# Optimization experiments

Measured on AMD Instinct MI355X. Metric: run time of the kernel, lower is better.

## Reference

```python
import jax, jax.numpy as jnp
import numpy as np

N = 20000
E = 320000
DIN = 256
DH = 64
DOUT = 64
H = 8
NEG_SLOPE = 0.2


def _glorot(key, shape):
    fan_in, fan_out = shape[0], shape[-1]
    lim = jnp.sqrt(6.0 / (fan_in + fan_out))
    return jax.random.uniform(key, shape, jnp.float32, -lim, lim)


def setup_inputs() -> dict:
    key = jax.random.key(0)
    ks = jax.random.split(key, 12)
    x = jax.random.normal(ks[0], (N, DIN), jnp.float32)
    edge_index = jax.random.randint(ks[1], (2, E), 0, N, jnp.int32)
    # layer 1: dim_in -> heads*dim_h
    Wl1 = _glorot(ks[2], (DIN, H * DH));  bl1 = jnp.zeros((H * DH,), jnp.float32)
    Wr1 = _glorot(ks[3], (DIN, H * DH));  br1 = jnp.zeros((H * DH,), jnp.float32)
    att1 = _glorot(ks[4], (H, DH))
    bias1 = jnp.zeros((H * DH,), jnp.float32)
    # layer 2: heads*dim_h -> heads*dim_out
    Wl2 = _glorot(ks[5], (H * DH, H * DOUT)); bl2 = jnp.zeros((H * DOUT,), jnp.float32)
    Wr2 = _glorot(ks[6], (H * DH, H * DOUT)); br2 = jnp.zeros((H * DOUT,), jnp.float32)
    att2 = _glorot(ks[7], (H, DOUT))
    bias2 = jnp.zeros((H * DOUT,), jnp.float32)
    return dict(x=x, edge_index=edge_index, Wl1=Wl1, bl1=bl1, Wr1=Wr1, br1=br1,
                att1=att1, bias1=bias1, Wl2=Wl2, bl2=bl2, Wr2=Wr2, br2=br2,
                att2=att2, bias2=bias2)


def _gatv2(x, src, dst, Wl, bl, Wr, br, att, bias_out, heads, out_ch):
    n = x.shape[0]
    l = (x @ Wl + bl).reshape(n, heads, out_ch)   # source transform
    r = (x @ Wr + br).reshape(n, heads, out_ch)   # target transform
    # per-edge GATv2 score: att . LeakyReLU(l_j + r_i)
    e = jax.nn.leaky_relu(l[src] + r[dst], NEG_SLOPE)      # [E, H, C]
    logits = jnp.einsum('ehc,hc->eh', e, att)              # [E, H]
    # segmented softmax over incoming edges of each destination node
    m = jax.ops.segment_max(logits, dst, num_segments=n)   # [N, H]
    expd = jnp.exp(logits - m[dst])
    denom = jax.ops.segment_sum(expd, dst, num_segments=n)
    alpha = expd / denom[dst]                              # [E, H]
    msg = l[src] * alpha[:, :, None]                       # [E, H, C]
    out = jax.ops.segment_sum(msg, dst, num_segments=n)    # [N, H, C]
    return out.reshape(n, heads * out_ch) + bias_out


def reference(x, edge_index, Wl1, bl1, Wr1, br1, att1, bias1,
              Wl2, bl2, Wr2, br2, att2, bias2):
    n = x.shape[0]
    loops = jnp.arange(n, dtype=edge_index.dtype)
    src = jnp.concatenate([edge_index[0], loops])  # GATv2Conv adds self-loops
    dst = jnp.concatenate([edge_index[1], loops])
    # dropout is identity at inference
    h = _gatv2(x, src, dst, Wl1, bl1, Wr1, br1, att1, bias1, H, DH)
    h = jax.nn.elu(h)
    h = _gatv2(h, src, dst, Wl2, bl2, Wr2, br2, att2, bias2, H, DOUT)
    return h, jax.nn.log_softmax(h, axis=1)
```

## Files before the change

kernel.cpp:

```cpp
#include <hip/hip_runtime.h>
#include <math.h>

#define NN   20000
#define NE   320000
#define ET   (NE + NN)
#define CPAD 16
#define D_IN 256
#define DHID 512
#define NLR  1024
#define MPAD 20096
#define NROWP 157
#define NCOLP 8

typedef __attribute__((ext_vector_type(8))) short bf16x8;
typedef __attribute__((ext_vector_type(4))) float f32x4;

typedef __attribute__((address_space(3))) uint       lds_uint;
typedef __attribute__((address_space(1))) const uint gbl_uint;
#define ASYNC16(gp, lp) \
    __builtin_amdgcn_global_load_lds((gbl_uint*)(gp), (lds_uint*)(lp), 16, 0, 0)

__device__ __forceinline__ ushort f2bf(float f) {
    uint u = __float_as_uint(f);
    return (ushort)((u + 0x7fffu + ((u >> 16) & 1u)) >> 16);
}


#define N1Q ((long)MPAD * D_IN / 4)
#define N2Q ((long)(MPAD - NN) * DHID / 4)
#define PREP_BLKS ((int)((N1Q + N2Q + 255) / 256))
#define INIT_BLKS ((NN + 255) / 256)

__global__ __launch_bounds__(256) void k_prep(const float* __restrict__ x,
                                              ushort* __restrict__ a,
                                              int* __restrict__ count,
                                              int* __restrict__ csr_src) {
    int b = blockIdx.x;
    if (b < PREP_BLKS) {
        long t = (long)b * 256 + threadIdx.x;
        if (t < N1Q) {
            long e = t * 4;
            int row = (int)(e >> 8);
            float4 v = make_float4(0.f, 0.f, 0.f, 0.f);
            if (row < NN) v = *(const float4*)&x[e];
            ushort4 o;
            o.x = f2bf(v.x); o.y = f2bf(v.y); o.z = f2bf(v.z); o.w = f2bf(v.w);
            *(ushort4*)&a[e] = o;
        } else if (t < N1Q + N2Q) {
            long e = (t - N1Q) * 4 + (long)NN * DHID;
            ushort4 z = {0, 0, 0, 0};
            *(ushort4*)&a[e] = z;
        }
    } else {
        int i = (b - PREP_BLKS) * 256 + threadIdx.x;
        if (i < NN) count[i] = 1;
        if (i < CPAD) csr_src[ET + i] = 0;
    }
}


#define HIST_BLKS ((NE + 255) / 256)
#define TW_BLKS   1024

__global__ __launch_bounds__(256) void k_hist_tw(const int* __restrict__ dstv,
                                                 int* __restrict__ count,
                                                 const float* __restrict__ Wl1,
                                                 const float* __restrict__ Wr1,
                                                 ushort* __restrict__ Wt1,
                                                 const float* __restrict__ Wl2,
                                                 const float* __restrict__ Wr2,
                                                 ushort* __restrict__ Wt2) {
    __shared__ float tile[32][33];
    int b = blockIdx.x;
    if (b < HIST_BLKS) {
        int e = b * 256 + threadIdx.x;
        if (e < NE) atomicAdd(&count[dstv[e]], 1);
        return;
    }
    int idx = b - HIST_BLKS;
    int z = idx >> 9;
    int rem = idx & 511;
    int K = z ? DHID : D_IN;
    int k0 = (rem & 15) * 32;
    if (k0 >= K) return;
    int n0 = (rem >> 4) * 32;
    int tx = threadIdx.x & 31, ty = threadIdx.x >> 5;
    const float* __restrict__ W = (n0 < DHID) ? (z ? Wl2 : Wl1) : (z ? Wr2 : Wr1);
    ushort* __restrict__ Wt = z ? Wt2 : Wt1;
    int nb = (n0 < DHID) ? n0 : n0 - DHID;
#pragma unroll
    for (int r = ty; r < 32; r += 8)
        tile[r][tx] = W[(long)(k0 + r) * DHID + nb + tx];
    __syncthreads();
#pragma unroll
    for (int r = ty; r < 32; r += 8)
        Wt[(long)(n0 + r) * K + k0 + tx] = f2bf(tile[tx][r]);
}


__global__ __launch_bounds__(1024) void scan_kernel(const int* __restrict__ count,
                                                    int* __restrict__ offs,
                                                    int* __restrict__ cursor) {
    __shared__ int sm[1024];
    const int CH = 20;
    int t = threadIdx.x;
    int base = t * CH;
    int local[CH];
    int s = 0;
#pragma unroll
    for (int i = 0; i < CH; i++) {
        int idx = base + i;
        int v = (idx < NN) ? count[idx] : 0;
        local[i] = s;
        s += v;
    }
    sm[t] = s;
    __syncthreads();
    for (int o = 1; o < 1024; o <<= 1) {
        int v = (t >= o) ? sm[t - o] : 0;
        __syncthreads();
        sm[t] += v;
        __syncthreads();
    }
    int pref = (t > 0) ? sm[t - 1] : 0;
#pragma unroll
    for (int i = 0; i < CH; i++) {
        int idx = base + i;
        if (idx < NN) {
            int o_ = pref + local[i];
            offs[idx] = o_;
            cursor[idx] = o_;
        }
    }
    if (t == 1023) offs[NN] = sm[1023];
}


#define BM 128
#define BN 128
#define BK 64
#define GEMM_BLKS (NROWP * NCOLP)
#define SCAT_BLKS ((ET + 255) / 256)

__global__ __launch_bounds__(256) void k_gemm_scatter(const ushort* __restrict__ A, int K,
                                                      const ushort* __restrict__ Wt,
                                                      const float* __restrict__ bl,
                                                      const float* __restrict__ br,
                                                      ushort* __restrict__ out,
                                                      const int* __restrict__ srcv,
                                                      const int* __restrict__ dstv,
                                                      int* __restrict__ cursor,
                                                      int* __restrict__ csr_src) {
    __shared__ ushort As[BM * BK];
    __shared__ ushort Bs[BN * BK];

    int bid = blockIdx.x;
    if (bid >= GEMM_BLKS) {
        int e = (bid - GEMM_BLKS) * 256 + threadIdx.x;
        if (e >= ET) return;
        int s, d;
        if (e < NE) { s = srcv[e]; d = dstv[e]; }
        else        { s = e - NE;  d = s; }
        int pos = atomicAdd(&cursor[d], 1);
        csr_src[pos] = s;
        return;
    }

    int t = threadIdx.x;
    int xcd = bid & 7;
    int idx = bid >> 3;
    int gl = xcd * NROWP + idx;
    int row0 = (gl >> 3) * BM;
    int col0 = (gl & 7) * BN;

    int lane = t & 63, w = t >> 6;
    int wr = w >> 1, wc = w & 1;
    int l16 = lane & 15, lhi = lane >> 4;

    f32x4 acc[4][4];
#pragma unroll
    for (int m = 0; m < 4; m++)
#pragma unroll
        for (int n = 0; n < 4; n++)
            acc[m][n] = (f32x4){0.f, 0.f, 0.f, 0.f};

    for (int k0 = 0; k0 < K; k0 += BK) {
#pragma unroll
        for (int q = 0; q < 4; q++) {
            int chunk = q * 256 + t;
            int row = chunk >> 3;
            int il = (chunk & 7) ^ (row & 7);
            ASYNC16(A  + (long)(row0 + row) * K + k0 + il * 8, (char*)As + chunk * 16);
            ASYNC16(Wt + (long)(col0 + row) * K + k0 + il * 8, (char*)Bs + chunk * 16);
        }
        __syncthreads();
#pragma unroll
        for (int kk = 0; kk < 2; kk++) {
            bf16x8 af[4], bfr[4];
#pragma unroll
            for (int m = 0; m < 4; m++) {
                int rl = wr * 64 + m * 16 + l16;
                int off = rl * 128 + ((kk * 64 + lhi * 16) ^ ((rl & 7) << 4));
                af[m] = *(const bf16x8*)((const char*)As + off);
            }
#pragma unroll
            for (int n = 0; n < 4; n++) {
                int rl = wc * 64 + n * 16 + l16;
                int off = rl * 128 + ((kk * 64 + lhi * 16) ^ ((rl & 7) << 4));
                bfr[n] = *(const bf16x8*)((const char*)Bs + off);
            }
#pragma unroll
            for (int m = 0; m < 4; m++)
#pragma unroll
                for (int n = 0; n < 4; n++)
                    acc[m][n] = __builtin_amdgcn_mfma_f32_16x16x32_bf16(bfr[n], af[m], acc[m][n], 0, 0, 0);
        }
        __syncthreads();
    }

    float4 bvn[4];
#pragma unroll
    for (int n = 0; n < 4; n++) {
        int colb = col0 + wc * 64 + n * 16 + lhi * 4;
        bvn[n] = (colb < DHID) ? *(const float4*)&bl[colb]
                               : *(const float4*)&br[colb - DHID];
    }
#pragma unroll
    for (int m = 0; m < 4; m++) {
        int row = row0 + wr * 64 + m * 16 + l16;
        if (row < NN) {
#pragma unroll
            for (int n = 0; n < 4; n++) {
                int colb = col0 + wc * 64 + n * 16 + lhi * 4;
                ushort4 p;
                p.x = f2bf(acc[m][n][0] + bvn[n].x);
                p.y = f2bf(acc[m][n][1] + bvn[n].y);
                p.z = f2bf(acc[m][n][2] + bvn[n].z);
                p.w = f2bf(acc[m][n][3] + bvn[n].w);
                *(ushort4*)&out[(long)row * NLR + colb] = p;
            }
        }
    }
}


#define CVT8(u, f)                                  \
    f[0] = __uint_as_float((u).x << 16);            \
    f[1] = __uint_as_float((u).x & 0xffff0000u);    \
    f[2] = __uint_as_float((u).y << 16);            \
    f[3] = __uint_as_float((u).y & 0xffff0000u);    \
    f[4] = __uint_as_float((u).z << 16);            \
    f[5] = __uint_as_float((u).z & 0xffff0000u);    \
    f[6] = __uint_as_float((u).w << 16);            \
    f[7] = __uint_as_float((u).w & 0xffff0000u);

template <int MODE>
__global__ __launch_bounds__(256) void aggregate_kernel(const ushort* __restrict__ lr,
                                                        const float* __restrict__ att,
                                                        const float* __restrict__ bias,
                                                        const int* __restrict__ csr_src,
                                                        const int* __restrict__ offs,
                                                        ushort* __restrict__ out_bf,
                                                        float* __restrict__ out_f32,
                                                        float* __restrict__ out_lsm) {
    int i = blockIdx.x * 4 + (threadIdx.x >> 6);
    int lane = threadIdx.x & 63;
    int c0 = lane << 3;

    uint4 ur = *(const uint4*)(lr + (long)i * NLR + DHID + c0);
    float rv[8];
    CVT8(ur, rv);
    float av[8];
    *(float4*)&av[0] = *(const float4*)&att[c0];
    *(float4*)&av[4] = *(const float4*)&att[c0 + 4];

    int beg = offs[i], end = offs[i + 1];
    float m = -3.0e38f, d = 0.f;
    float acc[8] = {0.f, 0.f, 0.f, 0.f, 0.f, 0.f, 0.f, 0.f};

    int j = csr_src[beg];
    uint4 v = *(const uint4*)(lr + (long)j * NLR + c0);

    for (int k = beg; k < end; k++) {
        uint4 vc = v;
        int kn = (k + 1 < end) ? k + 1 : k;
        int jn = csr_src[kn];
        v = *(const uint4*)(lr + (long)jn * NLR + c0);

        float lx[8];
        CVT8(vc, lx);
        float s = 0.f;
#pragma unroll
        for (int c = 0; c < 8; c++) {
            float e = lx[c] + rv[c];
            e = fmaxf(e, 0.2f * e);
            s = fmaf(av[c], e, s);
        }
        s *= 1.44269504f;
        s += __shfl_xor(s, 1);
        s += __shfl_xor(s, 2);
        s += __shfl_xor(s, 4);

        if (s > m) {
            float sc = exp2f(m - s);
            d *= sc;
#pragma unroll
            for (int c = 0; c < 8; c++) acc[c] *= sc;
            m = s;
        }
        float wgt = exp2f(s - m);
        d += wgt;
#pragma unroll
        for (int c = 0; c < 8; c++) acc[c] = fmaf(wgt, lx[c], acc[c]);
    }

    float inv = 1.f / d;
    float o[8];
    float4 bi0 = *(const float4*)&bias[c0];
    float4 bi1 = *(const float4*)&bias[c0 + 4];
    o[0] = fmaf(acc[0], inv, bi0.x); o[1] = fmaf(acc[1], inv, bi0.y);
    o[2] = fmaf(acc[2], inv, bi0.z); o[3] = fmaf(acc[3], inv, bi0.w);
    o[4] = fmaf(acc[4], inv, bi1.x); o[5] = fmaf(acc[5], inv, bi1.y);
    o[6] = fmaf(acc[6], inv, bi1.z); o[7] = fmaf(acc[7], inv, bi1.w);

    if (MODE == 0) {
#pragma unroll
        for (int c = 0; c < 8; c++) o[c] = (o[c] > 0.f) ? o[c] : expm1f(o[c]);
        uint4 p;
        p.x = (uint)f2bf(o[0]) | ((uint)f2bf(o[1]) << 16);
        p.y = (uint)f2bf(o[2]) | ((uint)f2bf(o[3]) << 16);
        p.z = (uint)f2bf(o[4]) | ((uint)f2bf(o[5]) << 16);
        p.w = (uint)f2bf(o[6]) | ((uint)f2bf(o[7]) << 16);
        *(uint4*)(out_bf + (long)i * DHID + c0) = p;
    } else {
        *(float4*)&out_f32[(long)i * DHID + c0]     = *(float4*)&o[0];
        *(float4*)&out_f32[(long)i * DHID + c0 + 4] = *(float4*)&o[4];
        float mx = o[0];
#pragma unroll
        for (int c = 1; c < 8; c++) mx = fmaxf(mx, o[c]);
#pragma unroll
        for (int off = 1; off < 64; off <<= 1) mx = fmaxf(mx, __shfl_xor(mx, off));
        float se = 0.f;
#pragma unroll
        for (int c = 0; c < 8; c++) se += __expf(o[c] - mx);
#pragma unroll
        for (int off = 1; off < 64; off <<= 1) se += __shfl_xor(se, off);
        float lg = mx + logf(se);
        float l0[8];
#pragma unroll
        for (int c = 0; c < 8; c++) l0[c] = o[c] - lg;
        *(float4*)&out_lsm[(long)i * DHID + c0]     = *(float4*)&l0[0];
        *(float4*)&out_lsm[(long)i * DHID + c0 + 4] = *(float4*)&l0[4];
    }
}


extern "C" void kernel_launch(void* const* d_in, const int* in_sizes, int n_in,
                              void* d_out, int out_size, void* d_ws, size_t ws_size,
                              hipStream_t stream) {
    const float* x     = (const float*)d_in[0];
    const int*   ei    = (const int*)d_in[1];
    const float* Wl1   = (const float*)d_in[2];
    const float* bl1   = (const float*)d_in[3];
    const float* Wr1   = (const float*)d_in[4];
    const float* br1   = (const float*)d_in[5];
    const float* att1  = (const float*)d_in[6];
    const float* bias1 = (const float*)d_in[7];
    const float* Wl2   = (const float*)d_in[8];
    const float* bl2   = (const float*)d_in[9];
    const float* Wr2   = (const float*)d_in[10];
    const float* br2   = (const float*)d_in[11];
    const float* att2  = (const float*)d_in[12];
    const float* bias2 = (const float*)d_in[13];

    float* out = (float*)d_out;
    float* h2  = out;
    float* lsm = out + (long)NN * DHID;

    ushort* lrbuf  = (ushort*)d_ws;
    ushort* Abf    = lrbuf + (long)NN * NLR;
    ushort* Wt1    = Abf + (long)MPAD * DHID;
    ushort* Wt2    = Wt1 + (long)NLR * D_IN;
    int*    csr_src = (int*)(Wt2 + (long)NLR * DHID);
    int*    count   = csr_src + ET + CPAD;
    int*    offs    = count + NN;
    int*    cursor  = offs + NN + 1;

    const int* srcv = ei;
    const int* dstv = ei + NE;

    k_prep<<<PREP_BLKS + INIT_BLKS, 256, 0, stream>>>(x, Abf, count, csr_src);
    k_hist_tw<<<HIST_BLKS + TW_BLKS, 256, 0, stream>>>(dstv, count, Wl1, Wr1, Wt1,
                                                       Wl2, Wr2, Wt2);
    scan_kernel<<<1, 1024, 0, stream>>>(count, offs, cursor);

    k_gemm_scatter<<<GEMM_BLKS + SCAT_BLKS, 256, 0, stream>>>(Abf, D_IN, Wt1, bl1, br1,
                                                              lrbuf, srcv, dstv, cursor, csr_src);
    aggregate_kernel<0><<<NN / 4, 256, 0, stream>>>(lrbuf, att1, bias1, csr_src, offs, Abf, nullptr, nullptr);

    k_gemm_scatter<<<GEMM_BLKS, 256, 0, stream>>>(Abf, DHID, Wt2, bl2, br2,
                                                  lrbuf, nullptr, nullptr, nullptr, nullptr);
    aggregate_kernel<1><<<NN / 4, 256, 0, stream>>>(lrbuf, att2, bias2, csr_src, offs, nullptr, h2, lsm);
}
```

Before: 254.7 us.

## Overlap layer-1 aggregation tail with layer-2 GEMM panels and merge prep kernels

```diff
diff --git a/kernel.cpp b/kernel.cpp
--- a/kernel.cpp
+++ b/kernel.cpp
@@ -12,6 +12,20 @@
 #define NROWP 157
 #define NCOLP 8
 
+#define BM 128
+#define BN 128
+#define BK 64
+#define GEMM_BLKS (NROWP * NCOLP)
+#define SCAT_BLKS ((ET + 255) / 256)
+
+#define A1_NODES 12032
+#define NB_A1 (A1_NODES / 4)
+#define NB_A2 ((NN - A1_NODES) / 4)
+#define G1_PANELS 94
+#define G2_PANELS (NROWP - G1_PANELS)
+#define NB_G1 (G1_PANELS * 8)
+#define NB_G2 (G2_PANELS * 8)
+
 typedef __attribute__((ext_vector_type(8))) short bf16x8;
 typedef __attribute__((ext_vector_type(4))) float f32x4;
 
@@ -25,16 +39,35 @@
     return (ushort)((u + 0x7fffu + ((u >> 16) & 1u)) >> 16);
 }
 
+#define CVT8(u, f)                                  \
+    f[0] = __uint_as_float((u).x << 16);            \
+    f[1] = __uint_as_float((u).x & 0xffff0000u);    \
+    f[2] = __uint_as_float((u).y << 16);            \
+    f[3] = __uint_as_float((u).y & 0xffff0000u);    \
+    f[4] = __uint_as_float((u).z << 16);            \
+    f[5] = __uint_as_float((u).z & 0xffff0000u);    \
+    f[6] = __uint_as_float((u).w << 16);            \
+    f[7] = __uint_as_float((u).w & 0xffff0000u);
+
 
 #define N1Q ((long)MPAD * D_IN / 4)
 #define N2Q ((long)(MPAD - NN) * DHID / 4)
 #define PREP_BLKS ((int)((N1Q + N2Q + 255) / 256))
-#define INIT_BLKS ((NN + 255) / 256)
-
-__global__ __launch_bounds__(256) void k_prep(const float* __restrict__ x,
-                                              ushort* __restrict__ a,
-                                              int* __restrict__ count,
-                                              int* __restrict__ csr_src) {
+#define HIST_BLKS ((NE + 255) / 256)
+#define TW_BLKS   1024
+
+__global__ __launch_bounds__(256) void k_prep_all(const float* __restrict__ x,
+                                                  ushort* __restrict__ a,
+                                                  const int* __restrict__ dstv,
+                                                  int* __restrict__ count,
+                                                  int* __restrict__ csr_src,
+                                                  const float* __restrict__ Wl1,
+                                                  const float* __restrict__ Wr1,
+                                                  ushort* __restrict__ Wt1,
+                                                  const float* __restrict__ Wl2,
+                                                  const float* __restrict__ Wr2,
+                                                  ushort* __restrict__ Wt2) {
+    __shared__ float tile[32][33];
     int b = blockIdx.x;
     if (b < PREP_BLKS) {
         long t = (long)b * 256 + threadIdx.x;
@@ -51,50 +84,36 @@
             ushort4 z = {0, 0, 0, 0};
             *(ushort4*)&a[e] = z;
         }
-    } else {
-        int i = (b - PREP_BLKS) * 256 + threadIdx.x;
-        if (i < NN) count[i] = 1;
-        if (i < CPAD) csr_src[ET + i] = 0;
-    }
-}
-
-
-#define HIST_BLKS ((NE + 255) / 256)
-#define TW_BLKS   1024
-
-__global__ __launch_bounds__(256) void k_hist_tw(const int* __restrict__ dstv,
-                                                 int* __restrict__ count,
-                                                 const float* __restrict__ Wl1,
-                                                 const float* __restrict__ Wr1,
-                                                 ushort* __restrict__ Wt1,
-                                                 const float* __restrict__ Wl2,
-                                                 const float* __restrict__ Wr2,
-                                                 ushort* __restrict__ Wt2) {
-    __shared__ float tile[32][33];
-    int b = blockIdx.x;
+        return;
+    }
+    b -= PREP_BLKS;
     if (b < HIST_BLKS) {
         int e = b * 256 + threadIdx.x;
         if (e < NE) atomicAdd(&count[dstv[e]], 1);
         return;
     }
-    int idx = b - HIST_BLKS;
-    int z = idx >> 9;
-    int rem = idx & 511;
-    int K = z ? DHID : D_IN;
-    int k0 = (rem & 15) * 32;
-    if (k0 >= K) return;
-    int n0 = (rem >> 4) * 32;
-    int tx = threadIdx.x & 31, ty = threadIdx.x >> 5;
-    const float* __restrict__ W = (n0 < DHID) ? (z ? Wl2 : Wl1) : (z ? Wr2 : Wr1);
-    ushort* __restrict__ Wt = z ? Wt2 : Wt1;
-    int nb = (n0 < DHID) ? n0 : n0 - DHID;
-#pragma unroll
-    for (int r = ty; r < 32; r += 8)
-        tile[r][tx] = W[(long)(k0 + r) * DHID + nb + tx];
-    __syncthreads();
-#pragma unroll
-    for (int r = ty; r < 32; r += 8)
-        Wt[(long)(n0 + r) * K + k0 + tx] = f2bf(tile[tx][r]);
+    b -= HIST_BLKS;
+    if (b < TW_BLKS) {
+        int z = b >> 9;
+        int rem = b & 511;
+        int K = z ? DHID : D_IN;
+        int k0 = (rem & 15) * 32;
+        if (k0 >= K) return;
+        int n0 = (rem >> 4) * 32;
+        int tx = threadIdx.x & 31, ty = threadIdx.x >> 5;
+        const float* __restrict__ W = (n0 < DHID) ? (z ? Wl2 : Wl1) : (z ? Wr2 : Wr1);
+        ushort* __restrict__ Wt = z ? Wt2 : Wt1;
+        int nb = (n0 < DHID) ? n0 : n0 - DHID;
+#pragma unroll
+        for (int r = ty; r < 32; r += 8)
+            tile[r][tx] = W[(long)(k0 + r) * DHID + nb + tx];
+        __syncthreads();
+#pragma unroll
+        for (int r = ty; r < 32; r += 8)
+            Wt[(long)(n0 + r) * K + k0 + tx] = f2bf(tile[tx][r]);
+        return;
+    }
+    if (threadIdx.x < CPAD) csr_src[ET + threadIdx.x] = 0;
 }
 
 
@@ -110,7 +129,7 @@
 #pragma unroll
     for (int i = 0; i < CH; i++) {
         int idx = base + i;
-        int v = (idx < NN) ? count[idx] : 0;
+        int v = (idx < NN) ? count[idx] + 1 : 0;
         local[i] = s;
         s += v;
     }
@@ -136,41 +155,18 @@
 }
 
 
-#define BM 128
-#define BN 128
-#define BK 64
-#define GEMM_BLKS (NROWP * NCOLP)
-#define SCAT_BLKS ((ET + 255) / 256)
-
-__global__ __launch_bounds__(256) void k_gemm_scatter(const ushort* __restrict__ A, int K,
-                                                      const ushort* __restrict__ Wt,
-                                                      const float* __restrict__ bl,
-                                                      const float* __restrict__ br,
-                                                      ushort* __restrict__ out,
-                                                      const int* __restrict__ srcv,
-                                                      const int* __restrict__ dstv,
-                                                      int* __restrict__ cursor,
-                                                      int* __restrict__ csr_src) {
-    __shared__ ushort As[BM * BK];
-    __shared__ ushort Bs[BN * BK];
-
-    int bid = blockIdx.x;
-    if (bid >= GEMM_BLKS) {
-        int e = (bid - GEMM_BLKS) * 256 + threadIdx.x;
-        if (e >= ET) return;
-        int s, d;
-        if (e < NE) { s = srcv[e]; d = dstv[e]; }
-        else        { s = e - NE;  d = s; }
-        int pos = atomicAdd(&cursor[d], 1);
-        csr_src[pos] = s;
-        return;
-    }
-
+__device__ __forceinline__ void gemm_body(const ushort* __restrict__ A, int K,
+                                          const ushort* __restrict__ Wt,
+                                          const float* __restrict__ bl,
+                                          const float* __restrict__ br,
+                                          ushort* __restrict__ out,
+                                          ushort* As, ushort* Bs,
+                                          int gi, int panel_base, int npanels) {
     int t = threadIdx.x;
-    int xcd = bid & 7;
-    int idx = bid >> 3;
-    int gl = xcd * NROWP + idx;
-    int row0 = (gl >> 3) * BM;
+    int xcd = gi & 7;
+    int idx = gi >> 3;
+    int gl = xcd * npanels + idx;
+    int row0 = (panel_base + (gl >> 3)) * BM;
     int col0 = (gl & 7) * BN;
 
     int lane = t & 63, w = t >> 6;
@@ -244,26 +240,17 @@
 }
 
 
-#define CVT8(u, f)                                  \
-    f[0] = __uint_as_float((u).x << 16);            \
-    f[1] = __uint_as_float((u).x & 0xffff0000u);    \
-    f[2] = __uint_as_float((u).y << 16);            \
-    f[3] = __uint_as_float((u).y & 0xffff0000u);    \
-    f[4] = __uint_as_float((u).z << 16);            \
-    f[5] = __uint_as_float((u).z & 0xffff0000u);    \
-    f[6] = __uint_as_float((u).w << 16);            \
-    f[7] = __uint_as_float((u).w & 0xffff0000u);
-
 template <int MODE>
-__global__ __launch_bounds__(256) void aggregate_kernel(const ushort* __restrict__ lr,
-                                                        const float* __restrict__ att,
-                                                        const float* __restrict__ bias,
-                                                        const int* __restrict__ csr_src,
-                                                        const int* __restrict__ offs,
-                                                        ushort* __restrict__ out_bf,
-                                                        float* __restrict__ out_f32,
-                                                        float* __restrict__ out_lsm) {
-    int i = blockIdx.x * 4 + (threadIdx.x >> 6);
+__device__ __forceinline__ void agg_body(const ushort* __restrict__ lr,
+                                         const float* __restrict__ att,
+                                         const float* __restrict__ bias,
+                                         const int* __restrict__ csr_src,
+                                         const int* __restrict__ offs,
+                                         ushort* __restrict__ out_bf,
+                                         float* __restrict__ out_f32,
+                                         float* __restrict__ out_lsm,
+                                         int node_base, int blk) {
+    int i = node_base + blk * 4 + ((int)threadIdx.x >> 6);
     int lane = threadIdx.x & 63;
     int c0 = lane << 3;
 
@@ -352,6 +339,85 @@
         *(float4*)&out_lsm[(long)i * DHID + c0]     = *(float4*)&l0[0];
         *(float4*)&out_lsm[(long)i * DHID + c0 + 4] = *(float4*)&l0[4];
     }
+}
+
+
+__global__ __launch_bounds__(256) void k_gemm1_scatter(const ushort* __restrict__ A,
+                                                       const ushort* __restrict__ Wt,
+                                                       const float* __restrict__ bl,
+                                                       const float* __restrict__ br,
+                                                       ushort* __restrict__ out,
+                                                       const int* __restrict__ srcv,
+                                                       const int* __restrict__ dstv,
+                                                       int* __restrict__ cursor,
+                                                       int* __restrict__ csr_src) {
+    __shared__ ushort As[BM * BK];
+    __shared__ ushort Bs[BN * BK];
+    const int TOT = GEMM_BLKS + SCAT_BLKS;
+    int bid = blockIdx.x;
+    int g0 = (int)(((long)bid * GEMM_BLKS) / TOT);
+    int g1 = (int)(((long)(bid + 1) * GEMM_BLKS) / TOT);
+    if (g1 > g0) {
+        gemm_body(A, D_IN, Wt, bl, br, out, As, Bs, g0, 0, NROWP);
+        return;
+    }
+    int e = (bid - g0) * 256 + threadIdx.x;
+    if (e >= ET) return;
+    int s, d;
+    if (e < NE) { s = srcv[e]; d = dstv[e]; }
+    else        { s = e - NE;  d = s; }
+    int pos = atomicAdd(&cursor[d], 1);
+    csr_src[pos] = s;
+}
+
+__global__ __launch_bounds__(256) void k_gemm(const ushort* __restrict__ A, int K,
+                                              const ushort* __restrict__ Wt,
+                                              const float* __restrict__ bl,
+                                              const float* __restrict__ br,
+                                              ushort* __restrict__ out,
+                                              int panel_base, int npanels) {
+    __shared__ ushort As[BM * BK];
+    __shared__ ushort Bs[BN * BK];
+    gemm_body(A, K, Wt, bl, br, out, As, Bs, blockIdx.x, panel_base, npanels);
+}
+
+template <int MODE>
+__global__ __launch_bounds__(256) void aggregate_kernel(const ushort* __restrict__ lr,
+                                                        const float* __restrict__ att,
+                                                        const float* __restrict__ bias,
+                                                        const int* __restrict__ csr_src,
+                                                        const int* __restrict__ offs,
+                                                        ushort* __restrict__ out_bf,
+                                                        float* __restrict__ out_f32,
+                                                        float* __restrict__ out_lsm,
+                                                        int node_base) {
+    agg_body<MODE>(lr, att, bias, csr_src, offs, out_bf, out_f32, out_lsm,
+                   node_base, blockIdx.x);
+}
+
+__global__ __launch_bounds__(256) void k_agg0_gemm2(const ushort* __restrict__ lr1,
+                                                    const float* __restrict__ att1,
+                                                    const float* __restrict__ bias1,
+                                                    const int* __restrict__ csr_src,
+                                                    const int* __restrict__ offs,
+                                                    ushort* __restrict__ h1,
+                                                    const ushort* __restrict__ Ah1,
+                                                    const ushort* __restrict__ Wt2,
+                                                    const float* __restrict__ bl2,
+                                                    const float* __restrict__ br2,
+                                                    ushort* __restrict__ lr2) {
+    __shared__ ushort As[BM * BK];
+    __shared__ ushort Bs[BN * BK];
+    const int TOT = NB_A2 + NB_G1;
+    int bid = blockIdx.x;
+    int g0 = (int)(((long)bid * NB_G1) / TOT);
+    int g1 = (int)(((long)(bid + 1) * NB_G1) / TOT);
+    if (g1 > g0) {
+        gemm_body(Ah1, DHID, Wt2, bl2, br2, lr2, As, Bs, g0, 0, G1_PANELS);
+        return;
+    }
+    agg_body<0>(lr1, att1, bias1, csr_src, offs, h1, nullptr, nullptr,
+                A1_NODES, bid - g0);
 }
 
 
@@ -377,28 +443,45 @@
     float* h2  = out;
     float* lsm = out + (long)NN * DHID;
 
-    ushort* lrbuf  = (ushort*)d_ws;
-    ushort* Abf    = lrbuf + (long)NN * NLR;
-    ushort* Wt1    = Abf + (long)MPAD * DHID;
-    ushort* Wt2    = Wt1 + (long)NLR * D_IN;
+    ushort* lrbuf   = (ushort*)d_ws;
+    ushort* Abf     = lrbuf + (long)NN * NLR;
+    ushort* Wt1     = Abf + (long)MPAD * DHID;
+    ushort* Wt2     = Wt1 + (long)NLR * D_IN;
     int*    csr_src = (int*)(Wt2 + (long)NLR * DHID);
     int*    count   = csr_src + ET + CPAD;
     int*    offs    = count + NN;
     int*    cursor  = offs + NN + 1;
+    ushort* lr2_big = (ushort*)(cursor + NN);
+
+    size_t need_big = (size_t)((char*)(lr2_big + (long)NN * NLR) - (char*)d_ws);
+    bool   BIG = (ws_size >= need_big);
+    ushort* lr2 = BIG ? lr2_big : lrbuf;
 
     const int* srcv = ei;
     const int* dstv = ei + NE;
 
-    k_prep<<<PREP_BLKS + INIT_BLKS, 256, 0, stream>>>(x, Abf, count, csr_src);
-    k_hist_tw<<<HIST_BLKS + TW_BLKS, 256, 0, stream>>>(dstv, count, Wl1, Wr1, Wt1,
-                                                       Wl2, Wr2, Wt2);
+    hipMemsetAsync(count, 0, NN * sizeof(int), stream);
+
+    k_prep_all<<<PREP_BLKS + HIST_BLKS + TW_BLKS + 1, 256, 0, stream>>>(
+        x, Abf, dstv, count, csr_src, Wl1, Wr1, Wt1, Wl2, Wr2, Wt2);
     scan_kernel<<<1, 1024, 0, stream>>>(count, offs, cursor);
-
-    k_gemm_scatter<<<GEMM_BLKS + SCAT_BLKS, 256, 0, stream>>>(Abf, D_IN, Wt1, bl1, br1,
-                                                              lrbuf, srcv, dstv, cursor, csr_src);
-    aggregate_kernel<0><<<NN / 4, 256, 0, stream>>>(lrbuf, att1, bias1, csr_src, offs, Abf, nullptr, nullptr);
-
-    k_gemm_scatter<<<GEMM_BLKS, 256, 0, stream>>>(Abf, DHID, Wt2, bl2, br2,
-                                                  lrbuf, nullptr, nullptr, nullptr, nullptr);
-    aggregate_kernel<1><<<NN / 4, 256, 0, stream>>>(lrbuf, att2, bias2, csr_src, offs, nullptr, h2, lsm);
-}
+    k_gemm1_scatter<<<GEMM_BLKS + SCAT_BLKS, 256, 0, stream>>>(
+        Abf, Wt1, bl1, br1, lrbuf, srcv, dstv, cursor, csr_src);
+
+    if (BIG) {
+        aggregate_kernel<0><<<NB_A1, 256, 0, stream>>>(
+            lrbuf, att1, bias1, csr_src, offs, Abf, nullptr, nullptr, 0);
+        k_agg0_gemm2<<<NB_A2 + NB_G1, 256, 0, stream>>>(
+            lrbuf, att1, bias1, csr_src, offs, Abf, Abf, Wt2, bl2, br2, lr2);
+        k_gemm<<<NB_G2, 256, 0, stream>>>(Abf, DHID, Wt2, bl2, br2, lr2,
+                                          G1_PANELS, G2_PANELS);
+    } else {
+        aggregate_kernel<0><<<NN / 4, 256, 0, stream>>>(
+            lrbuf, att1, bias1, csr_src, offs, Abf, nullptr, nullptr, 0);
+        k_gemm<<<GEMM_BLKS, 256, 0, stream>>>(Abf, DHID, Wt2, bl2, br2, lr2,
+                                              0, NROWP);
+    }
+
+    aggregate_kernel<1><<<NN / 4, 256, 0, stream>>>(
+        lr2, att2, bias2, csr_src, offs, nullptr, h2, lsm, 0);
+}
```

New measurement: 295.1 us. +15.9%, slower.
